# Optimization experiments

Hardware: AMD Instinct MI355X
Metric: run time of the kernel (lower is better)

Reference implementation:

```python
import jax, jax.numpy as jnp
import numpy as np

SIGMA = 32.0
EPS = 1e-8

def setup_inputs() -> dict:
    key = jax.random.key(0)
    k1, k2, k3 = jax.random.split(key, 3)
    N, D, O = 8192, 512, 512
    x = jax.random.normal(k1, (N, D), dtype=jnp.float32)
    # Linear params (kaiming-normal-ish init represented as scaled normals)
    W = jax.random.normal(k2, (O, D), dtype=jnp.float32) * (2.0 / D) ** 0.5
    b = jnp.zeros((O,), dtype=jnp.float32)
    return {"x": x, "W": W, "b": b}

def reference(x, W, b):
    # squared pairwise L2 distances via the Gram trick: ||xi||^2 + ||xj||^2 - 2 xi.xj
    sq = jnp.sum(x * x, axis=-1)                      # [N]
    sqd = sq[:, None] + sq[None, :] - 2.0 * (x @ x.T)  # [N, N]
    sqd = jnp.maximum(sqd, 0.0)                        # numerical clamp (cdist >= 0)
    weights = jnp.exp(-sqd / (2.0 * SIGMA * SIGMA))    # Gaussian kernel [N, N]
    weights = weights / (jnp.sum(weights, axis=1, keepdims=True) + EPS)
    output = weights @ x                               # Nadaraya-Watson weighted avg [N, D]
    return output @ W.T + b                            # linear head [N, O]
```

## Files before the change

kernel.cpp:

```cpp
#include <hip/hip_runtime.h>
#include <stdint.h>

#define NPTS 8192
#define DIM  512
#define ODIM 512

typedef __attribute__((ext_vector_type(8))) short short8;
typedef __attribute__((ext_vector_type(4))) float f32x4;

__device__ __forceinline__ void gload_lds16(const void* g, void* l) {
  __builtin_amdgcn_global_load_lds(
      (__attribute__((address_space(1))) void*)g,
      (__attribute__((address_space(3))) void*)l, 16, 0, 0);
}

__device__ __forceinline__ short f2bf(float f) {
  uint32_t u = __float_as_uint(f);
  u = (u + 0x7FFFu + ((u >> 16) & 1u)) >> 16;
  return (short)u;
}

#define VMB(N) do {                                          \
    asm volatile("s_waitcnt vmcnt(" #N ")" ::: "memory");    \
    __builtin_amdgcn_sched_barrier(0);                       \
    __builtin_amdgcn_s_barrier();                            \
    __builtin_amdgcn_sched_barrier(0);                       \
  } while (0)

__device__ __forceinline__ void gemm256_8ph(const short* __restrict__ A,
                                            const short* __restrict__ B,
                                            int K, int lda, int ldb,
                                            short* lds, f32x4 acc[8][4]) {
  const int tid = threadIdx.x, wid = tid >> 6, lane = tid & 63;
  const int wr = wid >> 2, wc = wid & 3, fr = lane & 15, fg = (lane >> 4) & 3;
  const int nt = K >> 6;
  const int rp = tid >> 3, slot = tid & 7;
  const int ch = slot ^ (rp & 7);

  const short* srcA[4]; const short* srcB[4];
#pragma unroll
  for (int u = 0; u < 4; ++u) {
    srcA[u] = A + (size_t)((u & 1) * 128 + (u >> 1) * 64 + rp) * lda + ch * 8;
    srcB[u] = B + (size_t)(((u * 2 + (rp >> 5)) & 3) * 64 + (u >> 1) * 32 + (rp & 31)) * ldb + ch * 8;
  }

  const int c0 = ((0 * 4 + fg) ^ (fr & 7)) * 8;
  const int c1 = ((1 * 4 + fg) ^ (fr & 7)) * 8;
  const int aRow = wr * 64 + fr;
  const int bRow = wc * 32 + fr;

#pragma unroll
  for (int s = 0; s < 2; ++s) gload_lds16(srcA[s], lds + s * 4096 + wid * 512);
#pragma unroll
  for (int s = 0; s < 2; ++s) gload_lds16(srcB[s], lds + 16384 + s * 4096 + wid * 512);
#pragma unroll
  for (int s = 2; s < 4; ++s) gload_lds16(srcB[s], lds + 16384 + s * 4096 + wid * 512);
#pragma unroll
  for (int s = 2; s < 4; ++s) gload_lds16(srcA[s], lds + s * 4096 + wid * 512);
  VMB(4);

  for (int t = 0; t < nt; ++t) {
    const int buf  = (t & 1) << 15;
    const int nbuf = buf ^ 32768;
    const bool pf  = (t + 1) < nt;
    const int k1   = (t + 1) << 6;
    const short* sA = lds + buf;
    const short* sB = lds + buf + 16384;
    short8 afA[4][2], afB[4][2], bb0[2][2], bb1[2][2];

#pragma unroll
    for (int m = 0; m < 4; ++m) {
      const int r = aRow + m * 16;
      afA[m][0] = *(const short8*)(sA + r * 64 + c0);
      afA[m][1] = *(const short8*)(sA + r * 64 + c1);
    }
#pragma unroll
    for (int n = 0; n < 2; ++n) {
      const int r = bRow + n * 16;
      bb0[n][0] = *(const short8*)(sB + r * 64 + c0);
      bb0[n][1] = *(const short8*)(sB + r * 64 + c1);
    }
    if (pf) {
#pragma unroll
      for (int s = 0; s < 2; ++s) gload_lds16(srcA[s] + k1, lds + nbuf + s * 4096 + wid * 512);
    }
    VMB(4);
    __builtin_amdgcn_s_setprio(1);
#pragma unroll
    for (int kk = 0; kk < 2; ++kk)
#pragma unroll
      for (int m = 0; m < 4; ++m)
#pragma unroll
        for (int n = 0; n < 2; ++n)
          acc[m][n] = __builtin_amdgcn_mfma_f32_16x16x32_bf16(afA[m][kk], bb0[n][kk], acc[m][n], 0, 0, 0);
    __builtin_amdgcn_s_setprio(0);

#pragma unroll
    for (int n = 0; n < 2; ++n) {
      const int r = 128 + bRow + n * 16;
      bb1[n][0] = *(const short8*)(sB + r * 64 + c0);
      bb1[n][1] = *(const short8*)(sB + r * 64 + c1);
    }
    if (pf) {
#pragma unroll
      for (int s = 0; s < 2; ++s) gload_lds16(srcB[s] + k1, lds + nbuf + 16384 + s * 4096 + wid * 512);
    }
    VMB(4);
    __builtin_amdgcn_s_setprio(1);
#pragma unroll
    for (int kk = 0; kk < 2; ++kk)
#pragma unroll
      for (int m = 0; m < 4; ++m)
#pragma unroll
        for (int n = 0; n < 2; ++n)
          acc[m][2 + n] = __builtin_amdgcn_mfma_f32_16x16x32_bf16(afA[m][kk], bb1[n][kk], acc[m][2 + n], 0, 0, 0);
    __builtin_amdgcn_s_setprio(0);

#pragma unroll
    for (int m = 0; m < 4; ++m) {
      const int r = 128 + aRow + m * 16;
      afB[m][0] = *(const short8*)(sA + r * 64 + c0);
      afB[m][1] = *(const short8*)(sA + r * 64 + c1);
    }
    if (pf) {
#pragma unroll
      for (int s = 2; s < 4; ++s) gload_lds16(srcB[s] + k1, lds + nbuf + 16384 + s * 4096 + wid * 512);
    }
    VMB(4);
    __builtin_amdgcn_s_setprio(1);
#pragma unroll
    for (int kk = 0; kk < 2; ++kk)
#pragma unroll
      for (int m = 0; m < 4; ++m)
#pragma unroll
        for (int n = 0; n < 2; ++n)
          acc[4 + m][2 + n] = __builtin_amdgcn_mfma_f32_16x16x32_bf16(afB[m][kk], bb1[n][kk], acc[4 + m][2 + n], 0, 0, 0);
    __builtin_amdgcn_s_setprio(0);

    if (pf) {
#pragma unroll
      for (int s = 2; s < 4; ++s) gload_lds16(srcA[s] + k1, lds + nbuf + s * 4096 + wid * 512);
    }
    VMB(4);
    __builtin_amdgcn_s_setprio(1);
#pragma unroll
    for (int kk = 0; kk < 2; ++kk)
#pragma unroll
      for (int m = 0; m < 4; ++m)
#pragma unroll
        for (int n = 0; n < 2; ++n)
          acc[4 + m][n] = __builtin_amdgcn_mfma_f32_16x16x32_bf16(afB[m][kk], bb0[n][kk], acc[4 + m][n], 0, 0, 0);
    __builtin_amdgcn_s_setprio(0);
  }
}

#define ZERO_ACC8(acc)                       \
  {                                          \
    f32x4 _z = {0.f, 0.f, 0.f, 0.f};         \
    _Pragma("unroll")                        \
    for (int m = 0; m < 8; ++m)              \
      _Pragma("unroll")                      \
      for (int n = 0; n < 4; ++n) acc[m][n] = _z; \
  }

__device__ __forceinline__ void gemm_core_nt(const short* __restrict__ A,
                                             const short* __restrict__ B,
                                             int K, int lda, int ldb,
                                             short* smem, f32x4 acc[4][4]) {
  const int tid  = threadIdx.x;
  const int wid  = tid >> 6;
  const int lane = tid & 63;
  const int wr = wid >> 1, wc = wid & 1;
  const int sr = lane >> 2;
  const int sc = (lane & 3) << 3;
  const int fr = lane & 15, fg = lane >> 4;
  short* sA = smem;
  short* sB = smem + 4096;
  short* dA0 = sA + wid * 512;
  short* dA1 = sA + 2048 + wid * 512;
  short* dB0 = sB + wid * 512;
  short* dB1 = sB + 2048 + wid * 512;
  const short* pa0 = A + (size_t)(wid * 16 + sr) * lda + sc;
  const short* pa1 = A + (size_t)(64 + wid * 16 + sr) * lda + sc;
  const short* pb0 = B + (size_t)(wid * 16 + sr) * ldb + sc;
  const short* pb1 = B + (size_t)(64 + wid * 16 + sr) * ldb + sc;

  for (int k0 = 0; k0 < K; k0 += 32) {
    gload_lds16(pa0 + k0, dA0);
    gload_lds16(pa1 + k0, dA1);
    gload_lds16(pb0 + k0, dB0);
    gload_lds16(pb1 + k0, dB1);
    __syncthreads();
    short8 af[4], bb[4];
#pragma unroll
    for (int m = 0; m < 4; ++m)
      af[m] = *(const short8*)(sA + (wr * 64 + m * 16 + fr) * 32 + fg * 8);
#pragma unroll
    for (int n = 0; n < 4; ++n)
      bb[n] = *(const short8*)(sB + (wc * 64 + n * 16 + fr) * 32 + fg * 8);
#pragma unroll
    for (int m = 0; m < 4; ++m)
#pragma unroll
      for (int n = 0; n < 4; ++n)
        acc[m][n] = __builtin_amdgcn_mfma_f32_16x16x32_bf16(af[m], bb[n], acc[m][n], 0, 0, 0);
    __syncthreads();
  }
}

#define ZERO_ACC4(acc)                       \
  {                                          \
    f32x4 _z = {0.f, 0.f, 0.f, 0.f};         \
    _Pragma("unroll")                        \
    for (int m = 0; m < 4; ++m)              \
      _Pragma("unroll")                      \
      for (int n = 0; n < 4; ++n) acc[m][n] = _z; \
  }

__global__ __launch_bounds__(256) void k_prep_x(const float* __restrict__ x,
                                                short* __restrict__ xb,
                                                float* __restrict__ sq) {
  const int row  = blockIdx.x * 4 + (threadIdx.x >> 6);
  const int lane = threadIdx.x & 63;
  const float* px = x + (size_t)row * DIM + lane * 8;
  const float4 v0 = *(const float4*)px;
  const float4 v1 = *(const float4*)(px + 4);
  float s = v0.x*v0.x + v0.y*v0.y + v0.z*v0.z + v0.w*v0.w +
            v1.x*v1.x + v1.y*v1.y + v1.z*v1.z + v1.w*v1.w;
  short8 o;
  o[0]=f2bf(v0.x); o[1]=f2bf(v0.y); o[2]=f2bf(v0.z); o[3]=f2bf(v0.w);
  o[4]=f2bf(v1.x); o[5]=f2bf(v1.y); o[6]=f2bf(v1.z); o[7]=f2bf(v1.w);
  *(short8*)(xb + (size_t)row * DIM + lane * 8) = o;
#pragma unroll
  for (int m = 32; m >= 1; m >>= 1) s += __shfl_xor(s, m);
  if (lane == 0) sq[row] = s;
}

__global__ __launch_bounds__(256) void k_prep_w(const float* __restrict__ W,
                                                short* __restrict__ Wb) {
  const int idx = blockIdx.x * 256 + threadIdx.x;
  const float4 v0 = *(const float4*)(W + (size_t)idx * 8);
  const float4 v1 = *(const float4*)(W + (size_t)idx * 8 + 4);
  short8 o;
  o[0]=f2bf(v0.x); o[1]=f2bf(v0.y); o[2]=f2bf(v0.z); o[3]=f2bf(v0.w);
  o[4]=f2bf(v1.x); o[5]=f2bf(v1.y); o[6]=f2bf(v1.z); o[7]=f2bf(v1.w);
  *(short8*)(Wb + (size_t)idx * 8) = o;
}

__global__ __launch_bounds__(256) void k_ybt(const short* __restrict__ xb,
                                             const short* __restrict__ Wb,
                                             short* __restrict__ YbT) {
  __shared__ short smem[8192];
  f32x4 acc[4][4];
  ZERO_ACC4(acc);
  const int rowBase = blockIdx.y * 128;
  const int colBase = blockIdx.x * 128;
  gemm_core_nt(Wb + (size_t)rowBase * DIM, xb + (size_t)colBase * DIM,
               DIM, DIM, DIM, smem, acc);
  const int lane = threadIdx.x & 63, wid = threadIdx.x >> 6;
  const int wr = wid >> 1, wc = wid & 1, fr = lane & 15, fg = lane >> 4;
#pragma unroll
  for (int m = 0; m < 4; ++m)
#pragma unroll
    for (int n = 0; n < 4; ++n)
#pragma unroll
      for (int r = 0; r < 4; ++r) {
        const int ro = rowBase + wr * 64 + m * 16 + fg * 4 + r;
        const int ci = colBase + wc * 64 + n * 16 + fr;
        YbT[(size_t)ro * NPTS + ci] = f2bf(acc[m][n][r]);
      }
}

__global__ __launch_bounds__(512, 2) void k_pmat(const short* __restrict__ xb,
                                                 const float* __restrict__ sq,
                                                 short* __restrict__ P,
                                                 float* __restrict__ rowsum,
                                                 int jbase, int SW) {
  __shared__ short lds[65536];
  f32x4 acc[8][4];
  ZERO_ACC8(acc);
  const int rowBase = blockIdx.y * 256;
  const int colTile = blockIdx.x * 256;
  const int jglob = jbase + colTile;
  gemm256_8ph(xb + (size_t)rowBase * DIM, xb + (size_t)jglob * DIM,
              DIM, DIM, DIM, lds, acc);
  const int lane = threadIdx.x & 63, wid = threadIdx.x >> 6;
  const int wr = wid >> 2, wc = wid & 3, fr = lane & 15, fg = lane >> 4;
  float sj[4];
#pragma unroll
  for (int n = 0; n < 4; ++n) sj[n] = sq[jglob + wc * 64 + n * 16 + fr];
#pragma unroll
  for (int m = 0; m < 8; ++m) {
#pragma unroll
    for (int r = 0; r < 4; ++r) {
      const int i = rowBase + wr * 128 + m * 16 + fg * 4 + r;
      const float si = sq[i];
      float rs = 0.f;
#pragma unroll
      for (int n = 0; n < 4; ++n) {
        const float t = fminf(2.f * acc[m][n][r] - si - sj[n], 0.f) * (1.0f / 2048.0f);
        const float w = __expf(t);
        rs += w;
        P[(size_t)i * SW + (colTile + wc * 64 + n * 16 + fr)] = f2bf(w);
      }
      rs += __shfl_xor(rs, 1);
      rs += __shfl_xor(rs, 2);
      rs += __shfl_xor(rs, 4);
      rs += __shfl_xor(rs, 8);
      if (fr == 0) atomicAdd(&rowsum[i], rs);
    }
  }
}

__global__ __launch_bounds__(512, 2) void k_pv(const short* __restrict__ P,
                                               const short* __restrict__ YbT,
                                               float* __restrict__ out_acc,
                                               int jbase, int SW, int klen) {
  __shared__ short lds[65536];
  f32x4 acc[8][4];
  ZERO_ACC8(acc);
  const int rowBase = blockIdx.y * 256;
  const int colBase = blockIdx.x * 256;
  const int kz = blockIdx.z * klen;
  gemm256_8ph(P + (size_t)rowBase * SW + kz,
              YbT + (size_t)colBase * NPTS + jbase + kz,
              klen, SW, NPTS, lds, acc);
  const int lane = threadIdx.x & 63, wid = threadIdx.x >> 6;
  const int wr = wid >> 2, wc = wid & 3, fr = lane & 15, fg = lane >> 4;
#pragma unroll
  for (int m = 0; m < 8; ++m)
#pragma unroll
    for (int n = 0; n < 4; ++n)
#pragma unroll
      for (int r = 0; r < 4; ++r) {
        const int i = rowBase + wr * 128 + m * 16 + fg * 4 + r;
        const int o = colBase + wc * 64 + n * 16 + fr;
        atomicAdd(&out_acc[(size_t)i * ODIM + o], acc[m][n][r]);
      }
}

__global__ __launch_bounds__(256) void k_final(const float* __restrict__ out_acc,
                                               const float* __restrict__ rowsum,
                                               const float* __restrict__ bvec,
                                               float* __restrict__ out) {
  const int idx = blockIdx.x * 256 + threadIdx.x;
  const int i = idx >> 7;
  const int o = (idx & 127) << 2;
  const float inv = 1.f / (rowsum[i] + 1e-8f);
  const float4 a = *(const float4*)(out_acc + (size_t)i * ODIM + o);
  const float4 bb = *(const float4*)(bvec + o);
  float4 r;
  r.x = a.x * inv + bb.x;
  r.y = a.y * inv + bb.y;
  r.z = a.z * inv + bb.z;
  r.w = a.w * inv + bb.w;
  *(float4*)(out + (size_t)i * ODIM + o) = r;
}

extern "C" void kernel_launch(void* const* d_in, const int* in_sizes, int n_in,
                              void* d_out, int out_size, void* d_ws, size_t ws_size,
                              hipStream_t stream) {
  (void)in_sizes; (void)n_in; (void)out_size;
  const float* x = (const float*)d_in[0];
  const float* W = (const float*)d_in[1];
  const float* bvec = (const float*)d_in[2];
  float* out = (float*)d_out;
  char* ws = (char*)d_ws;

  short* xb      = (short*)(ws + 0);
  short* Wb      = (short*)(ws + 8388608);
  short* YbT     = (short*)(ws + 8912896);
  float* sq      = (float*)(ws + 17301504);
  float* rowsum  = (float*)(ws + 17334272);
  float* out_acc = (float*)(ws + 17367040);
  short* P       = (short*)(ws + 34144256);

  size_t pav = ws_size > 34144256 ? ws_size - 34144256 : 0;
  int SW = 8192;
  while (SW > 256 && (size_t)NPTS * SW * 2 > pav) SW >>= 1;
  const int nstrips = NPTS / SW;
  int ksplit = SW / 2048;
  if (ksplit < 1) ksplit = 1;
  if (ksplit > 4) ksplit = 4;
  const int klen = SW / ksplit;

  hipMemsetAsync(rowsum, 0, NPTS * sizeof(float), stream);
  hipMemsetAsync(out_acc, 0, (size_t)NPTS * ODIM * sizeof(float), stream);

  k_prep_x<<<dim3(NPTS / 4), 256, 0, stream>>>(x, xb, sq);
  k_prep_w<<<dim3(ODIM * DIM / 8 / 256), 256, 0, stream>>>(W, Wb);
  k_ybt<<<dim3(NPTS / 128, ODIM / 128), 256, 0, stream>>>(xb, Wb, YbT);

  for (int s = 0; s < nstrips; ++s) {
    const int jbase = s * SW;
    k_pmat<<<dim3(SW / 256, NPTS / 256), 512, 0, stream>>>(xb, sq, P, rowsum, jbase, SW);
    k_pv<<<dim3(ODIM / 256, NPTS / 256, ksplit), 512, 0, stream>>>(P, YbT, out_acc, jbase, SW, klen);
  }

  k_final<<<dim3(NPTS * ODIM / 4 / 256), 256, 0, stream>>>(out_acc, rowsum, bvec, out);
}
```

Before: 331.2 us.

## Stage P tiles through LDS for coalesced stores and remap blocks across XCDs

The P-matrix epilogue now writes bf16 weights into swizzled LDS and then does 16-byte coalesced row stores to global memory, replacing the scattered 2-byte stores. Both k_pmat and k_pv remap their linear block index so that neighbouring tiles sharing operands land on the same XCD, which is meant to improve L2 reuse. The k_pmat remap hardcodes 32 column tiles and 8 XCDs, so it is only correct when SW is 8192. It also adds a barrier and reuses the GEMM's LDS buffer.

```diff
diff --git a/kernel.cpp b/kernel.cpp
--- a/kernel.cpp
+++ b/kernel.cpp
@@ -44,8 +44,8 @@
     srcB[u] = B + (size_t)(((u * 2 + (rp >> 5)) & 3) * 64 + (u >> 1) * 32 + (rp & 31)) * ldb + ch * 8;
   }
 
-  const int c0 = ((0 * 4 + fg) ^ (fr & 7)) * 8;
-  const int c1 = ((1 * 4 + fg) ^ (fr & 7)) * 8;
+  const int c0 = (fg ^ (fr & 7)) * 8;
+  const int c1 = ((4 + fg) ^ (fr & 7)) * 8;
   const int aRow = wr * 64 + fr;
   const int bRow = wc * 32 + fr;
 
@@ -278,12 +278,17 @@
   __shared__ short lds[65536];
   f32x4 acc[8][4];
   ZERO_ACC8(acc);
-  const int rowBase = blockIdx.y * 256;
-  const int colTile = blockIdx.x * 256;
+  const int n_lin = blockIdx.y * gridDim.x + blockIdx.x;
+  const int xcd = n_lin & 7, jj = n_lin >> 3;
+  const int bx = (xcd << 2) | (jj & 3);
+  const int by = jj >> 2;
+  const int rowBase = by * 256;
+  const int colTile = bx * 256;
   const int jglob = jbase + colTile;
   gemm256_8ph(xb + (size_t)rowBase * DIM, xb + (size_t)jglob * DIM,
               DIM, DIM, DIM, lds, acc);
   const int lane = threadIdx.x & 63, wid = threadIdx.x >> 6;
+  const int tid = threadIdx.x;
   const int wr = wid >> 2, wc = wid & 3, fr = lane & 15, fg = lane >> 4;
   float sj[4];
 #pragma unroll
@@ -293,14 +298,16 @@
 #pragma unroll
     for (int r = 0; r < 4; ++r) {
       const int i = rowBase + wr * 128 + m * 16 + fg * 4 + r;
+      const int iloc = wr * 128 + m * 16 + fg * 4 + r;
       const float si = sq[i];
       float rs = 0.f;
 #pragma unroll
-      for (int n = 0; n < 4; ++n) {
-        const float t = fminf(2.f * acc[m][n][r] - si - sj[n], 0.f) * (1.0f / 2048.0f);
+      for (int nn = 0; nn < 4; ++nn) {
+        const float t = fminf(2.f * acc[m][nn][r] - si - sj[nn], 0.f) * (1.0f / 2048.0f);
         const float w = __expf(t);
         rs += w;
-        P[(size_t)i * SW + (colTile + wc * 64 + n * 16 + fr)] = f2bf(w);
+        const int pc = (wc * 8 + nn * 2 + (fr >> 3)) ^ ((iloc >> 2) & 3);
+        lds[iloc * 256 + pc * 8 + (fr & 7)] = f2bf(w);
       }
       rs += __shfl_xor(rs, 1);
       rs += __shfl_xor(rs, 2);
@@ -309,18 +316,37 @@
       if (fr == 0) atomicAdd(&rowsum[i], rs);
     }
   }
+  __syncthreads();
+#pragma unroll
+  for (int v = 0; v < 16; ++v) {
+    const int gc = v * 512 + tid;
+    const int i = gc >> 5, c = gc & 31;
+    const int pc = c ^ ((i >> 2) & 3);
+    short8 val = *(const short8*)(lds + i * 256 + pc * 8);
+    *(short8*)(P + (size_t)(rowBase + i) * SW + colTile + c * 8) = val;
+  }
 }
 
 __global__ __launch_bounds__(512, 2) void k_pv(const short* __restrict__ P,
                                                const short* __restrict__ YbT,
                                                float* __restrict__ out_acc,
-                                               int jbase, int SW, int klen) {
+                                               int jbase, int SW, int klen,
+                                               int nz) {
   __shared__ short lds[65536];
   f32x4 acc[8][4];
   ZERO_ACC8(acc);
-  const int rowBase = blockIdx.y * 256;
-  const int colBase = blockIdx.x * 256;
-  const int kz = blockIdx.z * klen;
+  const int n_lin = (blockIdx.z * gridDim.y + blockIdx.y) * gridDim.x + blockIdx.x;
+  int bx, by, bz;
+  if (nz == 4) {
+    bx = n_lin & 1;
+    bz = (n_lin >> 1) & 3;
+    by = n_lin >> 3;
+  } else {
+    bx = blockIdx.x; by = blockIdx.y; bz = blockIdx.z;
+  }
+  const int rowBase = by * 256;
+  const int colBase = bx * 256;
+  const int kz = bz * klen;
   gemm256_8ph(P + (size_t)rowBase * SW + kz,
               YbT + (size_t)colBase * NPTS + jbase + kz,
               klen, SW, NPTS, lds, acc);
@@ -393,7 +419,7 @@
   for (int s = 0; s < nstrips; ++s) {
     const int jbase = s * SW;
     k_pmat<<<dim3(SW / 256, NPTS / 256), 512, 0, stream>>>(xb, sq, P, rowsum, jbase, SW);
-    k_pv<<<dim3(ODIM / 256, NPTS / 256, ksplit), 512, 0, stream>>>(P, YbT, out_acc, jbase, SW, klen);
+    k_pv<<<dim3(ODIM / 256, NPTS / 256, ksplit), 512, 0, stream>>>(P, YbT, out_acc, jbase, SW, klen, ksplit);
   }
 
   k_final<<<dim3(NPTS * ODIM / 4 / 256), 256, 0, stream>>>(out_acc, rowsum, bvec, out);
```

New measurement: 327.0 us. No clear change (-1.3%).

## Exploit kernel-matrix symmetry in P computation and retile PV GEMM to 128x128

Applied to the files above, without the earlier changes.

The weight matrix is symmetric, so when the full strip fits (SW == 8192) the P kernel now computes only upper-triangular 256x256 tiles (528 blocks) and writes each off-diagonal tile twice, once directly and once transposed through LDS. Column sums of mirrored tiles are added atomically to rowsum. P stores are staged through swizzled LDS so they go out as coalesced 16-byte writes. The PV GEMM moves to a simpler 128x128 single-buffered tile with 256 threads and a remapped block order, trading pipelining for more blocks and occupancy. The transposed write gathers scalar LDS reads, which adds epilogue cost.

```diff
diff --git a/kernel.cpp b/kernel.cpp
--- a/kernel.cpp
+++ b/kernel.cpp
@@ -44,8 +44,8 @@
     srcB[u] = B + (size_t)(((u * 2 + (rp >> 5)) & 3) * 64 + (u >> 1) * 32 + (rp & 31)) * ldb + ch * 8;
   }
 
-  const int c0 = ((0 * 4 + fg) ^ (fr & 7)) * 8;
-  const int c1 = ((1 * 4 + fg) ^ (fr & 7)) * 8;
+  const int c0 = (fg ^ (fr & 7)) * 8;
+  const int c1 = ((4 + fg) ^ (fr & 7)) * 8;
   const int aRow = wr * 64 + fr;
   const int bRow = wc * 32 + fr;
 
@@ -159,6 +159,67 @@
     f32x4 _z = {0.f, 0.f, 0.f, 0.f};         \
     _Pragma("unroll")                        \
     for (int m = 0; m < 8; ++m)              \
+      _Pragma("unroll")                      \
+      for (int n = 0; n < 4; ++n) acc[m][n] = _z; \
+  }
+
+__device__ __forceinline__ void gemm128(const short* __restrict__ A,
+                                        const short* __restrict__ B,
+                                        int K, int lda, int ldb,
+                                        short* lds, f32x4 acc[4][4]) {
+  const int tid = threadIdx.x, wid = tid >> 6, lane = tid & 63;
+  const int wr = wid >> 1, wc = wid & 1, fr = lane & 15, fg = (lane >> 4) & 3;
+  const int nt = K >> 6;
+  const short* srcA[4]; const short* srcB[4]; int dst[4];
+#pragma unroll
+  for (int u = 0; u < 4; ++u) {
+    const int g = u * 256 + tid;
+    const int r = g >> 3;
+    const int cl = (g & 7) ^ (r & 7);
+    srcA[u] = A + (size_t)r * lda + cl * 8;
+    srcB[u] = B + (size_t)r * ldb + cl * 8;
+    dst[u] = (u * 256 + wid * 64) * 8;
+  }
+  short* sB = lds + 8192;
+  const int c0 = (fg ^ (fr & 7)) * 8;
+  const int c1 = ((4 + fg) ^ (fr & 7)) * 8;
+
+  for (int t = 0; t < nt; ++t) {
+    const int k0 = t << 6;
+#pragma unroll
+    for (int u = 0; u < 4; ++u) gload_lds16(srcA[u] + k0, lds + dst[u]);
+#pragma unroll
+    for (int u = 0; u < 4; ++u) gload_lds16(srcB[u] + k0, sB + dst[u]);
+    __syncthreads();
+    short8 af[4][2], bb[4][2];
+#pragma unroll
+    for (int m = 0; m < 4; ++m) {
+      const int rr = (wr * 64 + m * 16 + fr) * 64;
+      af[m][0] = *(const short8*)(lds + rr + c0);
+      af[m][1] = *(const short8*)(lds + rr + c1);
+    }
+#pragma unroll
+    for (int n = 0; n < 4; ++n) {
+      const int rr = (wc * 64 + n * 16 + fr) * 64;
+      bb[n][0] = *(const short8*)(sB + rr + c0);
+      bb[n][1] = *(const short8*)(sB + rr + c1);
+    }
+#pragma unroll
+    for (int kk = 0; kk < 2; ++kk)
+#pragma unroll
+      for (int m = 0; m < 4; ++m)
+#pragma unroll
+        for (int n = 0; n < 4; ++n)
+          acc[m][n] = __builtin_amdgcn_mfma_f32_16x16x32_bf16(af[m][kk], bb[n][kk], acc[m][n], 0, 0, 0);
+    __syncthreads();
+  }
+}
+
+#define ZERO_ACC4(acc)                       \
+  {                                          \
+    f32x4 _z = {0.f, 0.f, 0.f, 0.f};         \
+    _Pragma("unroll")                        \
+    for (int m = 0; m < 4; ++m)              \
       _Pragma("unroll")                      \
       for (int n = 0; n < 4; ++n) acc[m][n] = _z; \
   }
@@ -207,15 +268,6 @@
   }
 }
 
-#define ZERO_ACC4(acc)                       \
-  {                                          \
-    f32x4 _z = {0.f, 0.f, 0.f, 0.f};         \
-    _Pragma("unroll")                        \
-    for (int m = 0; m < 4; ++m)              \
-      _Pragma("unroll")                      \
-      for (int n = 0; n < 4; ++n) acc[m][n] = _z; \
-  }
-
 __global__ __launch_bounds__(256) void k_prep_x(const float* __restrict__ x,
                                                 short* __restrict__ xb,
                                                 float* __restrict__ sq) {
@@ -278,29 +330,46 @@
   __shared__ short lds[65536];
   f32x4 acc[8][4];
   ZERO_ACC8(acc);
-  const int rowBase = blockIdx.y * 256;
-  const int colTile = blockIdx.x * 256;
-  const int jglob = jbase + colTile;
+  int bi, bj; bool mirror;
+  if (gridDim.y > 1) {
+    bi = blockIdx.y; bj = blockIdx.x; mirror = false;
+  } else {
+    int n = blockIdx.x; bi = 0;
+    while (n >= 32 - bi) { n -= 32 - bi; ++bi; }
+    bj = bi + n; mirror = (bj != bi);
+  }
+  const int rowBase = bi * 256;
+  const int colOff  = bj * 256;
+  const int jglob   = jbase + colOff;
   gemm256_8ph(xb + (size_t)rowBase * DIM, xb + (size_t)jglob * DIM,
               DIM, DIM, DIM, lds, acc);
-  const int lane = threadIdx.x & 63, wid = threadIdx.x >> 6;
-  const int wr = wid >> 2, wc = wid & 3, fr = lane & 15, fg = lane >> 4;
-  float sj[4];
-#pragma unroll
-  for (int n = 0; n < 4; ++n) sj[n] = sq[jglob + wc * 64 + n * 16 + fr];
+  const int tid = threadIdx.x, lane = tid & 63, wid = tid >> 6;
+  const int wr = wid >> 2, wc = wid & 3, fr = lane & 15, fg = (lane >> 4) & 3;
+  float sjv[4];
+#pragma unroll
+  for (int n = 0; n < 4; ++n) sjv[n] = sq[jglob + wc * 64 + n * 16 + fr];
+  float cs[4] = {0.f, 0.f, 0.f, 0.f};
 #pragma unroll
   for (int m = 0; m < 8; ++m) {
 #pragma unroll
     for (int r = 0; r < 4; ++r) {
-      const int i = rowBase + wr * 128 + m * 16 + fg * 4 + r;
+      const int il = wr * 128 + m * 16 + fg * 4 + r;
+      const int i  = rowBase + il;
       const float si = sq[i];
       float rs = 0.f;
 #pragma unroll
       for (int n = 0; n < 4; ++n) {
-        const float t = fminf(2.f * acc[m][n][r] - si - sj[n], 0.f) * (1.0f / 2048.0f);
+        const int jl = wc * 64 + n * 16 + fr;
+        const float t = fminf(2.f * acc[m][n][r] - si - sjv[n], 0.f) * (1.0f / 2048.0f);
         const float w = __expf(t);
-        rs += w;
-        P[(size_t)i * SW + (colTile + wc * 64 + n * 16 + fr)] = f2bf(w);
+        rs += w; cs[n] += w;
+        const float wo = __shfl_xor(w, 1);
+        if ((fr & 1) == 0) {
+          const uint32_t pair = (uint32_t)(uint16_t)f2bf(w) |
+                                ((uint32_t)(uint16_t)f2bf(wo) << 16);
+          const int pc = (jl >> 3) ^ ((il >> 3) & 7);
+          *(uint32_t*)&lds[il * 256 + pc * 8 + (jl & 7)] = pair;
+        }
       }
       rs += __shfl_xor(rs, 1);
       rs += __shfl_xor(rs, 2);
@@ -309,30 +378,71 @@
       if (fr == 0) atomicAdd(&rowsum[i], rs);
     }
   }
-}
-
-__global__ __launch_bounds__(512, 2) void k_pv(const short* __restrict__ P,
-                                               const short* __restrict__ YbT,
-                                               float* __restrict__ out_acc,
-                                               int jbase, int SW, int klen) {
-  __shared__ short lds[65536];
-  f32x4 acc[8][4];
-  ZERO_ACC8(acc);
-  const int rowBase = blockIdx.y * 256;
-  const int colBase = blockIdx.x * 256;
-  const int kz = blockIdx.z * klen;
-  gemm256_8ph(P + (size_t)rowBase * SW + kz,
-              YbT + (size_t)colBase * NPTS + jbase + kz,
-              klen, SW, NPTS, lds, acc);
+  if (mirror) {
+#pragma unroll
+    for (int n = 0; n < 4; ++n) {
+      cs[n] += __shfl_xor(cs[n], 16);
+      cs[n] += __shfl_xor(cs[n], 32);
+    }
+    if (lane < 16) {
+#pragma unroll
+      for (int n = 0; n < 4; ++n)
+        atomicAdd(&rowsum[jglob + wc * 64 + n * 16 + lane], cs[n]);
+    }
+  }
+  __syncthreads();
+#pragma unroll
+  for (int v = 0; v < 16; ++v) {
+    const int g = v * 512 + tid;
+    const int rl = g >> 5, c = g & 31;
+    const int pc = c ^ ((rl >> 3) & 7);
+    short8 val = *(const short8*)(lds + rl * 256 + pc * 8);
+    *(short8*)(P + (size_t)(rowBase + rl) * SW + colOff + c * 8) = val;
+  }
+  if (mirror) {
+#pragma unroll
+    for (int v = 0; v < 16; ++v) {
+      const int g = v * 512 + tid;
+      const int jl = g >> 5, ci = g & 31;
+      short8 o;
+#pragma unroll
+      for (int e = 0; e < 8; ++e)
+        o[e] = lds[(ci * 8 + e) * 256 + (((jl >> 3) ^ (ci & 7)) << 3) + (jl & 7)];
+      *(short8*)(P + (size_t)(jglob + jl) * SW + rowBase + ci * 8) = o;
+    }
+  }
+}
+
+__global__ __launch_bounds__(256) void k_pv(const short* __restrict__ P,
+                                            const short* __restrict__ YbT,
+                                            float* __restrict__ out_acc,
+                                            int jbase, int SW, int klen) {
+  __shared__ short lds[16384];
+  f32x4 acc[4][4];
+  ZERO_ACC4(acc);
+  int bx = blockIdx.x, by = blockIdx.y, bz = blockIdx.z;
+  if (gridDim.x == 4 && gridDim.y == 64 && gridDim.z == 4) {
+    const int n = blockIdx.x + blockIdx.y * 4 + blockIdx.z * 256;
+    const int low3 = n & 7, rest = n >> 3;
+    bx = rest & 3;
+    const int q = ((rest >> 2) << 3) | low3;
+    by = q >> 2; bz = q & 3;
+  }
+  const int rowBase = by * 128;
+  const int colBase = bx * 128;
+  const int kz = bz * klen;
+  gemm128(P + (size_t)rowBase * SW + kz,
+          YbT + (size_t)colBase * NPTS + jbase + kz,
+          klen, SW, NPTS, lds, acc);
   const int lane = threadIdx.x & 63, wid = threadIdx.x >> 6;
-  const int wr = wid >> 2, wc = wid & 3, fr = lane & 15, fg = lane >> 4;
-#pragma unroll
-  for (int m = 0; m < 8; ++m)
+  const int wr = wid >> 1, wc = wid & 1, fr = lane & 15, fg = (lane >> 4) & 3;
+#pragma unroll
+  for (int m = 0; m < 4; ++m)
 #pragma unroll
     for (int n = 0; n < 4; ++n)
 #pragma unroll
       for (int r = 0; r < 4; ++r) {
-        const int i = rowBase + wr * 128 + m * 16 + fg * 4 + r;
+        const int i = rowBase + wr * 64 + m * 16 + fg * 4 + r;
         const int o = colBase + wc * 64 + n * 16 + fr;
         atomicAdd(&out_acc[(size_t)i * ODIM + o], acc[m][n][r]);
       }
@@ -392,8 +502,12 @@
 
   for (int s = 0; s < nstrips; ++s) {
     const int jbase = s * SW;
-    k_pmat<<<dim3(SW / 256, NPTS / 256), 512, 0, stream>>>(xb, sq, P, rowsum, jbase, SW);
-    k_pv<<<dim3(ODIM / 256, NPTS / 256, ksplit), 512, 0, stream>>>(P, YbT, out_acc, jbase, SW, klen);
+    if (SW == 8192) {
+      k_pmat<<<dim3(528, 1), 512, 0, stream>>>(xb, sq, P, rowsum, 0, SW);
+    } else {
+      k_pmat<<<dim3(SW / 256, NPTS / 256), 512, 0, stream>>>(xb, sq, P, rowsum, jbase, SW);
+    }
+    k_pv<<<dim3(ODIM / 128, NPTS / 128, ksplit), 256, 0, stream>>>(P, YbT, out_acc, jbase, SW, klen);
   }
 
   k_final<<<dim3(NPTS * ODIM / 4 / 256), 256, 0, stream>>>(out_acc, rowsum, bvec, out);
```

New measurement: 337.7 us. About the same (+2.0%).
